# Optimization experiments

Measured on AMD Instinct MI355X. Metric: run time of the kernel, lower is better.

Reference implementation:

```python
import jax, jax.numpy as jnp
import numpy as np
from jax import lax

R = 10          # 10 iterations of (3x3x3 conv > 0) == one binary box dilation of radius 10
TOP_N = 250
SMOOTH = 1e-5
WEIGHT_CE = 1.0
WEIGHT_DICE = 1.0
FR_WEIGHT = 5.0


def _box_dilate(mask, r=R):
    # binary dilation with a (2r+1)^3 box, done separably along D,H,W
    x = mask.astype(jnp.float32)
    for axis in (1, 2, 3):
        win = [1, 1, 1, 1]
        win[axis] = 2 * r + 1
        x = lax.reduce_window(x, 0.0, lax.max, tuple(win), (1, 1, 1, 1), 'SAME')
    return x > 0


def _masked_mean(x, mask):
    cnt = jnp.sum(mask)
    s = jnp.sum(jnp.where(mask, x, 0.0))
    return jnp.where(cnt > 0, s / jnp.maximum(cnt, 1), 0.0)


def _fr_loss(feature, label):
    pos = label[:, 0] == 1                                  # (B,D,H,W)
    neg = label[:, 0] == 0
    f = jnp.moveaxis(feature, 1, -1)                        # (B,D,H,W,C)
    cnt = jnp.sum(pos)
    # mean positive feature (zeros if no positives)
    mean_pos = jnp.sum(jnp.where(pos[..., None], f, 0.0), axis=(0, 1, 2, 3)) / jnp.maximum(cnt, 1)
    std_feat = jnp.where(cnt > 0, mean_pos, 0.0)
    std_n = std_feat / jnp.maximum(jnp.linalg.norm(std_feat), 1e-12)
    # normalized feature map; cosine of a normalized feature with std_n == dot product
    f_n = f / jnp.maximum(jnp.linalg.norm(f, axis=-1, keepdims=True), 1e-12)
    cos_map = jnp.einsum('bdhwc,c->bdhw', f_n, std_n)
    # 1) positive compactness loss
    positive_loss = _masked_mean(1.0 - cos_map, pos)
    easy = _box_dilate(pos) & (~pos)
    mis_loss = _masked_mean(jax.nn.relu(cos_map), easy)
    # 3) hardest negatives: top-250 negative similarities, scatter to mask, dilate
    neg_sims = jnp.where(neg, cos_map, -1e30).reshape(-1)
    top_v, top_i = lax.top_k(neg_sims, TOP_N)
    hi = jnp.zeros(neg_sims.shape, jnp.float32).at[top_i].set((top_v > -1e29).astype(jnp.float32))
    hi = hi.reshape(pos.shape) > 0
    final_neg = _box_dilate(hi) & (~pos)
    neg_loss = _masked_mean(jax.nn.relu(cos_map), final_neg)
    return positive_loss + mis_loss + neg_loss


def _ce_and_dice(net_output, target):
    C = net_output.shape[1]
    logp = jax.nn.log_softmax(net_output, axis=1)           # (B,C,D,H,W)
    ce = -jnp.mean(jnp.take_along_axis(logp, target, axis=1))
    p = jnp.exp(logp)
    y = jax.nn.one_hot(target[:, 0], C, dtype=p.dtype)      # (B,D,H,W,C)
    y = jnp.moveaxis(y, -1, 1)                               # (B,C,D,H,W)
    axes = (0, 2, 3, 4)                                      # batch_dice=True
    tp = jnp.sum(p * y, axes)
    fp = jnp.sum(p * (1.0 - y), axes)
    fn = jnp.sum((1.0 - p) * y, axes)
    dc = (2.0 * tp + SMOOTH) / jnp.maximum(2.0 * tp + fp + fn + SMOOTH, 1e-8)
    dc_loss = -jnp.mean(dc[1:])                              # do_bg=False
    return ce, dc_loss


def setup_inputs() -> dict:
    key = jax.random.key(0)
    k1, k2, k3 = jax.random.split(key, 3)
    B, Cf, Cls, S = 2, 16, 3, 128
    feature = jax.random.normal(k1, (B, Cf, S, S, S), dtype=jnp.float32)
    net_output = jax.random.normal(k2, (B, Cls, S, S, S), dtype=jnp.float32)
    target = jax.random.randint(k3, (B, 1, S, S, S), 0, 3, dtype=jnp.int32)
    return {"feature": feature, "net_output": net_output, "target": target}


def reference(feature, net_output, target):
    ce, dc = _ce_and_dice(net_output, target)
    fr = _fr_loss(feature, target)
    return WEIGHT_CE * ce + WEIGHT_DICE * dc + FR_WEIGHT * fr
```

## Files before the change

kernel.cpp:

```cpp
#include <hip/hip_runtime.h>
#include <hip/hip_bf16.h>
#include <math.h>

#define S3    128
#define NB    2
#define CF    16
#define CHS   (S3*S3*S3)
#define NVOX  (NB*CHS)
#define NW    (NVOX/64)
#define CAP   1048576

typedef unsigned long long u64;
typedef unsigned int u32;
typedef float f4 __attribute__((ext_vector_type(4)));
typedef int   i4 __attribute__((ext_vector_type(4)));

#define ACC_OFF    0
#define STD_OFF    512
#define SCAN_OFF   576
#define HIST_OFF   1024
#define HIB_OFF    (HIST_OFF + 4096*4)
#define ZERO_BYTES (HIB_OFF + NW*8)
#define POSB_OFF   544768
#define NEGB_OFF   (POSB_OFF + NW*8)
#define DTMP_OFF   (NEGB_OFF + NW*8)
#define CAND_OFF   (DTMP_OFF + 2*NW*8)
#define COS_OFF    (CAND_OFF + CAP*8)


__device__ __forceinline__ double wave_red(double x) {
    for (int o = 32; o > 0; o >>= 1) x += __shfl_down(x, o);
    return x;
}
__device__ __forceinline__ u32 mono_key(float f) {
    u32 u = __float_as_uint(f);
    return (u & 0x80000000u) ? ~u : (u | 0x80000000u);
}
__device__ __forceinline__ u64 spread4(u32 x16) {
    u64 x = (u64)(x16 & 0xFFFFu);
    x = (x | (x << 24)) & 0x000000FF000000FFull;
    x = (x | (x << 12)) & 0x000F000F000F000Full;
    x = (x | (x << 6))  & 0x0303030303030303ull;
    x = (x | (x << 3))  & 0x1111111111111111ull;
    return x;
}

template<int NBINS>
__device__ __forceinline__ void sel_desc(const u32* h, u32 need, u32* ss, u32* res)
{
    const int t = threadIdx.x;
    const int CH = NBINS / 256;
    u32 s = 0;
    #pragma unroll
    for (int j = 0; j < CH; j++) s += h[t * CH + j];
    ss[t] = s;
    __syncthreads();
    for (int o = 1; o < 256; o <<= 1) {
        u32 v = (t + o < 256) ? ss[t + o] : 0;
        __syncthreads();
        ss[t] += v;
        __syncthreads();
    }
    u32 above = ss[t] - s;
    if (above < need && above + s >= need) {
        u32 cum = above;
        int bin = t * CH;
        for (int b = t * CH + CH - 1; b >= t * CH; b--) {
            if (cum + h[b] >= need) { bin = b; break; }
            cum += h[b];
        }
        res[0] = (u32)bin;
        res[1] = need - cum;
    }
    __syncthreads();
}

__global__ __launch_bounds__(256) void k_main(const float* __restrict__ feat,
        const float* __restrict__ net, const int* __restrict__ tgt,
        u64* __restrict__ posb, u64* __restrict__ negb, double* __restrict__ acc)
{
    int tid = blockIdx.x * 256 + threadIdx.x;
    const int gstride = gridDim.x * 256;
    const int lane = threadIdx.x & 63;
    float fs[16];
    #pragma unroll
    for (int c = 0; c < 16; c++) fs[c] = 0.f;
    float ce = 0.f, s0 = 0.f, s1 = 0.f, s2 = 0.f, ta0 = 0.f, ta1 = 0.f, ta2 = 0.f;
    int n0 = 0, n1 = 0, n2 = 0;

    for (int idx = tid; idx < NVOX / 4; idx += gstride) {
        const int v4 = idx << 2;
        const int b = v4 >> 21;
        const i4 tv = __builtin_nontemporal_load((const i4*)(tgt + v4));
        const int T[4] = {tv[0], tv[1], tv[2], tv[3]};
        u32 nib_p = (u32)(T[0]==1) | ((u32)(T[1]==1)<<1) | ((u32)(T[2]==1)<<2) | ((u32)(T[3]==1)<<3);
        u32 nib_n = (u32)(T[0]==0) | ((u32)(T[1]==0)<<1) | ((u32)(T[2]==0)<<2) | ((u32)(T[3]==0)<<3);
        int pp = __popc(nib_p), nn_ = __popc(nib_n);
        n1 += pp; n0 += nn_; n2 += 4 - pp - nn_;

        u64 bp0 = __ballot(nib_p & 1), bp1 = __ballot(nib_p & 2),
            bp2 = __ballot(nib_p & 4), bp3 = __ballot(nib_p & 8);
        u64 bn0 = __ballot(nib_n & 1), bn1 = __ballot(nib_n & 2),
            bn2 = __ballot(nib_n & 4), bn3 = __ballot(nib_n & 8);
        if ((lane & 15) == 0) {
            int wsel = lane >> 4, sh = wsel << 4;
            u64 wp = spread4((u32)(bp0 >> sh)) | (spread4((u32)(bp1 >> sh)) << 1)
                   | (spread4((u32)(bp2 >> sh)) << 2) | (spread4((u32)(bp3 >> sh)) << 3);
            u64 wn = spread4((u32)(bn0 >> sh)) | (spread4((u32)(bn1 >> sh)) << 1)
                   | (spread4((u32)(bn2 >> sh)) << 2) | (spread4((u32)(bn3 >> sh)) << 3);
            int wi = ((idx - lane) >> 4) + wsel;
            posb[wi] = wp; negb[wi] = wn;
        }

        const size_t nbase = (size_t)v4 + (size_t)b * (2u * CHS);
        f4 a0 = __builtin_nontemporal_load((const f4*)(net + nbase));
        f4 a1 = __builtin_nontemporal_load((const f4*)(net + nbase + CHS));
        f4 a2 = __builtin_nontemporal_load((const f4*)(net + nbase + 2 * (size_t)CHS));
        #pragma unroll
        for (int j = 0; j < 4; j++) {
            float x0 = a0[j], x1 = a1[j], x2 = a2[j];
            float m = fmaxf(x0, fmaxf(x1, x2));
            float e0 = expf(x0 - m), e1 = expf(x1 - m), e2 = expf(x2 - m);
            float sum = e0 + e1 + e2;
            float lse = m + logf(sum);
            int t = T[j];
            float xt = (t == 0) ? x0 : ((t == 1) ? x1 : x2);
            ce += lse - xt;
            float inv = 1.f / sum;
            float p0 = e0 * inv, p1 = e1 * inv, p2 = e2 * inv;
            s0 += p0; s1 += p1; s2 += p2;
            if (t == 0) ta0 += p0; else if (t == 1) ta1 += p1; else ta2 += p2;
        }

        if (nib_p) {
            const float* fb = feat + (size_t)v4 + (size_t)b * ((size_t)(CF - 1) * CHS);
            float w0 = (float)(nib_p & 1), w1 = (float)((nib_p >> 1) & 1),
                  w2 = (float)((nib_p >> 2) & 1), w3 = (float)((nib_p >> 3) & 1);
            #pragma unroll
            for (int c = 0; c < 16; c++) {
                float4 f = *(const float4*)(fb + (size_t)c * CHS);
                fs[c] += f.x * w0 + f.y * w1 + f.z * w2 + f.w * w3;
            }
        }
    }

    __shared__ double red[4][26];
    double vals[26];
    #pragma unroll
    for (int c = 0; c < 16; c++) vals[c] = (double)fs[c];
    vals[16] = n0; vals[17] = n1; vals[18] = n2;
    vals[19] = ce; vals[20] = s0; vals[21] = s1; vals[22] = s2;
    vals[23] = ta0; vals[24] = ta1; vals[25] = ta2;
    int wid = threadIdx.x >> 6;
    #pragma unroll
    for (int i = 0; i < 26; i++) {
        double x = wave_red(vals[i]);
        if (lane == 0) red[wid][i] = x;
    }
    __syncthreads();
    if (threadIdx.x < 26) {
        double s = red[0][threadIdx.x] + red[1][threadIdx.x] + red[2][threadIdx.x] + red[3][threadIdx.x];
        atomicAdd(&acc[threadIdx.x], s);
    }
}

__global__ void k_std(const double* __restrict__ acc, float* __restrict__ stdn) {
    __shared__ float v[16];
    double cnt = acc[17];
    if (threadIdx.x < 16) {
        double mp = acc[threadIdx.x] / fmax(cnt, 1.0);
        v[threadIdx.x] = (cnt > 0.0) ? (float)mp : 0.0f;
    }
    __syncthreads();
    if (threadIdx.x == 0) {
        float n = 0;
        for (int c = 0; c < 16; c++) n += v[c] * v[c];
        n = fmaxf(sqrtf(n), 1e-12f);
        for (int c = 0; c < 16; c++) stdn[c] = v[c] / n;
    }
}

__global__ __launch_bounds__(256) void k_cos(const float* __restrict__ feat,
        const float* __restrict__ stdn, const u64* __restrict__ negb,
        float* __restrict__ cosm, u32* __restrict__ hist)
{
    __shared__ u32 h[4096];
    __shared__ float sn[16];
    for (int i = threadIdx.x; i < 4096; i += 256) h[i] = 0;
    if (threadIdx.x < 16) sn[threadIdx.x] = stdn[threadIdx.x];
    __syncthreads();
    int tid = blockIdx.x * 256 + threadIdx.x;
    const int gstride = gridDim.x * 256;
    for (int idx = tid; idx < NVOX / 4; idx += gstride) {
        const int v4 = idx << 2;
        const int b = v4 >> 21;
        const float* fb = feat + (size_t)v4 + (size_t)b * ((size_t)(CF - 1) * CHS);
        float d0 = 0, d1 = 0, d2 = 0, d3 = 0, q0 = 0, q1 = 0, q2 = 0, q3 = 0;
        #pragma unroll
        for (int c = 0; c < 16; c++) {
            float4 f = *(const float4*)(fb + (size_t)c * CHS);
            float s = sn[c];
            d0 = fmaf(f.x, s, d0); q0 = fmaf(f.x, f.x, q0);
            d1 = fmaf(f.y, s, d1); q1 = fmaf(f.y, f.y, q1);
            d2 = fmaf(f.z, s, d2); q2 = fmaf(f.z, f.z, q2);
            d3 = fmaf(f.w, s, d3); q3 = fmaf(f.w, f.w, q3);
        }
        f4 cv;
        cv[0] = d0 / fmaxf(sqrtf(q0), 1e-12f);
        cv[1] = d1 / fmaxf(sqrtf(q1), 1e-12f);
        cv[2] = d2 / fmaxf(sqrtf(q2), 1e-12f);
        cv[3] = d3 / fmaxf(sqrtf(q3), 1e-12f);
        __builtin_nontemporal_store(cv, (f4*)(cosm + v4));
        u32 nib = (u32)(negb[v4 >> 6] >> (v4 & 63)) & 0xFu;
        if (nib & 1) atomicAdd(&h[mono_key(cv[0]) >> 20], 1u);
        if (nib & 2) atomicAdd(&h[mono_key(cv[1]) >> 20], 1u);
        if (nib & 4) atomicAdd(&h[mono_key(cv[2]) >> 20], 1u);
        if (nib & 8) atomicAdd(&h[mono_key(cv[3]) >> 20], 1u);
    }
    __syncthreads();
    for (int i = threadIdx.x; i < 4096; i += 256)
        if (h[i]) atomicAdd(&hist[i], h[i]);
}

__global__ __launch_bounds__(256) void k_scanA(const u32* __restrict__ hist, u32* __restrict__ scan) {
    __shared__ u32 h[4096];
    __shared__ u32 ss[256];
    __shared__ u32 res[2];
    for (int i = threadIdx.x; i < 4096; i += 256) h[i] = hist[i];
    __syncthreads();
    sel_desc<4096>(h, 250u, ss, res);
    if (threadIdx.x == 0) { scan[0] = res[0]; scan[1] = res[1]; }
}

__global__ __launch_bounds__(256) void k_collect(const float* __restrict__ cosm,
        const u64* __restrict__ negb, u32* __restrict__ scan, u64* __restrict__ cand)
{
    const u32 thr = scan[0] << 20;
    int tid = blockIdx.x * 256 + threadIdx.x;
    const int gstride = gridDim.x * 256;
    for (int idx = tid; idx < NVOX / 4; idx += gstride) {
        const int v4 = idx << 2;
        u32 nib = (u32)(negb[v4 >> 6] >> (v4 & 63)) & 0xFu;
        if (!nib) continue;
        float4 cv = *(const float4*)(cosm + v4);
        const float C[4] = {cv.x, cv.y, cv.z, cv.w};
        #pragma unroll
        for (int j = 0; j < 4; j++) {
            if ((nib >> j) & 1) {
                u32 key = mono_key(C[j]);
                if (key >= thr) {
                    u32 p = atomicAdd(&scan[4], 1u);
                    if (p < CAP) cand[p] = ((u64)key << 32) | (u32)(v4 + j);
                }
            }
        }
    }
}

__global__ __launch_bounds__(256) void k_select(const u64* __restrict__ cand,
        const u32* __restrict__ scan, u64* __restrict__ hib)
{
    __shared__ u32 h[4096];
    __shared__ u32 ss[256];
    __shared__ u32 res[2];
    __shared__ u32 eqlist[2048];
    __shared__ u32 eqc;
    const u32 cnt = scan[4];
    const int n = (int)(cnt < CAP ? cnt : CAP);
    const u32 binA = scan[0];
    const u32 need1 = scan[1];

    for (int i = threadIdx.x; i < 4096; i += 256) h[i] = 0;
    if (threadIdx.x == 0) eqc = 0;
    __syncthreads();
    for (int i = threadIdx.x; i < n; i += 256) {
        u32 key = (u32)(cand[i] >> 32);
        if ((key >> 20) == binA) atomicAdd(&h[(key >> 8) & 0xFFFu], 1u);
    }
    __syncthreads();
    sel_desc<4096>(h, need1, ss, res);
    const u32 b1 = res[0], need2 = res[1];

    for (int i = threadIdx.x; i < 4096; i += 256) h[i] = 0;
    __syncthreads();
    const u32 pre24 = (binA << 12) | b1;
    for (int i = threadIdx.x; i < n; i += 256) {
        u32 key = (u32)(cand[i] >> 32);
        if ((key >> 8) == pre24) atomicAdd(&h[key & 0xFFu], 1u);
    }
    __syncthreads();
    sel_desc<256>(h, need2, ss, res);
    const u32 K = (pre24 << 8) | res[0];
    const u32 need3 = res[1];

    for (int i = threadIdx.x; i < n; i += 256) {
        u64 code = cand[i];
        u32 key = (u32)(code >> 32), vi = (u32)code;
        if (key > K) atomicOr(&hib[vi >> 6], 1ull << (vi & 63));
        else if (key == K) { u32 p = atomicAdd(&eqc, 1u); if (p < 2048) eqlist[p] = vi; }
    }
    __syncthreads();
    if (threadIdx.x == 0) {
        int m = (int)(eqc < 2048u ? eqc : 2048u);
        u32 prev = 0; bool first = true;
        for (u32 k = 0; k < need3; k++) {
            u32 best = 0xFFFFFFFFu;
            for (int i = 0; i < m; i++) {
                u32 x = eqlist[i];
                if ((first || x > prev) && x < best) best = x;
            }
            if (best == 0xFFFFFFFFu) break;
            atomicOr(&hib[best >> 6], 1ull << (best & 63));
            prev = best; first = false;
        }
    }
}

__global__ __launch_bounds__(256) void k_dilD(const u64* __restrict__ posb,
        const u64* __restrict__ hib, u64* __restrict__ dtmp)
{
    int t = blockIdx.x * 256 + threadIdx.x;
    int m = t >> 16, wI = t & 65535;
    const u64* in = m ? hib : posb;
    int dd = (wI >> 8) & 127;
    int base = wI - (dd << 8);
    int lo = dd > 10 ? dd - 10 : 0, hi2 = dd + 10 > 127 ? 127 : dd + 10;
    u64 r = 0;
    for (int j = lo; j <= hi2; j++) r |= in[base + (j << 8)];
    dtmp[t] = r;
}

__global__ __launch_bounds__(256) void k_dilfin(const u64* __restrict__ dtmp,
        const u64* __restrict__ posb, const float* __restrict__ cosm,
        double* __restrict__ acc)
{
    __shared__ u64 A0[256], A1[256], B0[256], B1[256], E[256], F[256], P[256];
    __shared__ double red[4][5];
    const int s = blockIdx.x;
    const int t = threadIdx.x;
    const int sbase = s * 256;
    A0[t] = dtmp[sbase + t];
    A1[t] = dtmp[65536 + sbase + t];
    P[t]  = posb[sbase + t];
    __syncthreads();
    {
        int hh = t >> 1, col = t & 1;
        int lo = hh > 10 ? hh - 10 : 0, hi2 = hh + 10 > 127 ? 127 : hh + 10;
        u64 r0 = 0, r1 = 0;
        for (int j = lo; j <= hi2; j++) { r0 |= A0[(j << 1) + col]; r1 |= A1[(j << 1) + col]; }
        B0[t] = r0; B1[t] = r1;
    }
    __syncthreads();
    if (t < 128) {
        u64 lo0 = B0[t * 2], hi0 = B0[t * 2 + 1];
        u64 lo1 = B1[t * 2], hi1 = B1[t * 2 + 1];
        u64 rl0 = lo0, rh0 = hi0, rl1 = lo1, rh1 = hi1;
        #pragma unroll
        for (int sft = 1; sft <= 10; sft++) {
            rl0 |= (lo0 << sft) | (lo0 >> sft) | (hi0 << (64 - sft));
            rh0 |= (hi0 << sft) | (hi0 >> sft) | (lo0 >> (64 - sft));
            rl1 |= (lo1 << sft) | (lo1 >> sft) | (hi1 << (64 - sft));
            rh1 |= (hi1 << sft) | (hi1 >> sft) | (lo1 >> (64 - sft));
        }
        E[t * 2] = rl0; E[t * 2 + 1] = rh0;
        F[t * 2] = rl1; F[t * 2 + 1] = rh1;
    }
    __syncthreads();
    float sp = 0.f, se = 0.f, sf = 0.f;
    int cE = 0, cF = 0;
    const float* cbase = cosm + (size_t)s * 16384;
    #pragma unroll 4
    for (int i = 0; i < 16; i++) {
        int q = t + 256 * i;
        int lw = q >> 4, sh = (q & 15) * 4;
        u64 pw = P[lw];
        u32 np_ = (u32)(pw >> sh) & 0xFu;
        u32 ne  = (u32)((E[lw] & ~pw) >> sh) & 0xFu;
        u32 nf  = (u32)((F[lw] & ~pw) >> sh) & 0xFu;
        if (!(np_ | ne | nf)) continue;
        f4 cv = __builtin_nontemporal_load((const f4*)(cbase + q * 4));
        #pragma unroll
        for (int j = 0; j < 4; j++) {
            float cs = cv[j], rl = fmaxf(cs, 0.f);
            if ((np_ >> j) & 1) sp += 1.f - cs;
            if ((ne >> j) & 1) { se += rl; cE++; }
            if ((nf >> j) & 1) { sf += rl; cF++; }
        }
    }
    int lane = t & 63, wid = t >> 6;
    double vals[5] = {(double)sp, (double)se, (double)cE, (double)sf, (double)cF};
    #pragma unroll
    for (int i = 0; i < 5; i++) {
        double x = wave_red(vals[i]);
        if (lane == 0) red[wid][i] = x;
    }
    __syncthreads();
    if (t < 5) {
        double sum = red[0][t] + red[1][t] + red[2][t] + red[3][t];
        atomicAdd(&acc[26 + t], sum);
    }
}

__global__ void k_combine(const double* __restrict__ acc, float* __restrict__ out) {
    if (threadIdx.x != 0 || blockIdx.x != 0) return;
    double ce = acc[19] / (double)NVOX;
    double dcl = 0;
    for (int c = 1; c <= 2; c++) {
        double T = acc[23 + c], S = acc[20 + c], N = acc[16 + c];
        dcl += (2.0 * T + 1e-5) / fmax(S + N + 1e-5, 1e-8);
    }
    double dc_loss = -(dcl / 2.0);
    double cnt = acc[17];
    double pl = (cnt > 0.0) ? acc[26] / fmax(cnt, 1.0) : 0.0;
    double ml = (acc[28] > 0.0) ? acc[27] / acc[28] : 0.0;
    double nl = (acc[30] > 0.0) ? acc[29] / acc[30] : 0.0;
    out[0] = (float)(ce + dc_loss + 5.0 * (pl + ml + nl));
}

extern "C" void kernel_launch(void* const* d_in, const int* in_sizes, int n_in,
                              void* d_out, int out_size, void* d_ws, size_t ws_size,
                              hipStream_t stream)
{
    const float* feat = (const float*)d_in[0];
    const float* net  = (const float*)d_in[1];
    const int*   tgt  = (const int*)d_in[2];
    float* out = (float*)d_out;
    char* w = (char*)d_ws;

    double* acc  = (double*)(w + ACC_OFF);
    float* stdn  = (float*)(w + STD_OFF);
    u32* scan    = (u32*)(w + SCAN_OFF);
    u32* hist    = (u32*)(w + HIST_OFF);
    u64* hib     = (u64*)(w + HIB_OFF);
    u64* posb    = (u64*)(w + POSB_OFF);
    u64* negb    = (u64*)(w + NEGB_OFF);
    u64* dtmp    = (u64*)(w + DTMP_OFF);
    u64* cand    = (u64*)(w + CAND_OFF);
    float* cosm  = (float*)(w + COS_OFF);

    hipMemsetAsync(w, 0, ZERO_BYTES, stream);

    k_main   <<<2048, 256, 0, stream>>>(feat, net, tgt, posb, negb, acc);
    k_std    <<<1,    64,  0, stream>>>(acc, stdn);
    k_cos    <<<2048, 256, 0, stream>>>(feat, stdn, negb, cosm, hist);
    k_scanA  <<<1,    256, 0, stream>>>(hist, scan);
    k_collect<<<2048, 256, 0, stream>>>(cosm, negb, scan, cand);
    k_select <<<1,    256, 0, stream>>>(cand, scan, hib);
    k_dilD   <<<512,  256, 0, stream>>>(posb, hib, dtmp);
    k_dilfin <<<256,  256, 0, stream>>>(dtmp, posb, cosm, acc);
    k_combine<<<1,    64,  0, stream>>>(acc, out);
}
```

Baseline: 197.6 us.

## Split positive-feature sum out of main kernel into separate dense pass

Splits the fused main kernel into a CE/dice/bitmask kernel and a separate kernel that sums positive-voxel features using the posb bitmask with branch-free weights. The goal is to remove the divergent conditional 16-channel feature loads and the register pressure of the fused kernel. In exchange it adds a kernel launch, and the new kernel reads all feature data unconditionally instead of only groups containing positives. With about a third of voxels positive, nearly every group was loading features anyway.

```diff
diff --git a/kernel.cpp b/kernel.cpp
--- a/kernel.cpp
+++ b/kernel.cpp
@@ -75,16 +75,13 @@
     __syncthreads();
 }
 
-__global__ __launch_bounds__(256) void k_main(const float* __restrict__ feat,
-        const float* __restrict__ net, const int* __restrict__ tgt,
-        u64* __restrict__ posb, u64* __restrict__ negb, double* __restrict__ acc)
+__global__ __launch_bounds__(256) void k_ce(const float* __restrict__ net,
+        const int* __restrict__ tgt, u64* __restrict__ posb, u64* __restrict__ negb,
+        double* __restrict__ acc)
 {
     int tid = blockIdx.x * 256 + threadIdx.x;
     const int gstride = gridDim.x * 256;
     const int lane = threadIdx.x & 63;
-    float fs[16];
-    #pragma unroll
-    for (int c = 0; c < 16; c++) fs[c] = 0.f;
     float ce = 0.f, s0 = 0.f, s1 = 0.f, s2 = 0.f, ta0 = 0.f, ta1 = 0.f, ta2 = 0.f;
     int n0 = 0, n1 = 0, n2 = 0;
 
@@ -131,34 +128,58 @@
             s0 += p0; s1 += p1; s2 += p2;
             if (t == 0) ta0 += p0; else if (t == 1) ta1 += p1; else ta2 += p2;
         }
-
-        if (nib_p) {
-            const float* fb = feat + (size_t)v4 + (size_t)b * ((size_t)(CF - 1) * CHS);
-            float w0 = (float)(nib_p & 1), w1 = (float)((nib_p >> 1) & 1),
-                  w2 = (float)((nib_p >> 2) & 1), w3 = (float)((nib_p >> 3) & 1);
-            #pragma unroll
-            for (int c = 0; c < 16; c++) {
-                float4 f = *(const float4*)(fb + (size_t)c * CHS);
-                fs[c] += f.x * w0 + f.y * w1 + f.z * w2 + f.w * w3;
-            }
-        }
-    }
-
-    __shared__ double red[4][26];
-    double vals[26];
-    #pragma unroll
-    for (int c = 0; c < 16; c++) vals[c] = (double)fs[c];
-    vals[16] = n0; vals[17] = n1; vals[18] = n2;
-    vals[19] = ce; vals[20] = s0; vals[21] = s1; vals[22] = s2;
-    vals[23] = ta0; vals[24] = ta1; vals[25] = ta2;
+    }
+
+    __shared__ double red[4][10];
+    double vals[10] = {(double)n0, (double)n1, (double)n2, (double)ce,
+                       (double)s0, (double)s1, (double)s2,
+                       (double)ta0, (double)ta1, (double)ta2};
     int wid = threadIdx.x >> 6;
     #pragma unroll
-    for (int i = 0; i < 26; i++) {
+    for (int i = 0; i < 10; i++) {
         double x = wave_red(vals[i]);
         if (lane == 0) red[wid][i] = x;
     }
     __syncthreads();
-    if (threadIdx.x < 26) {
+    if (threadIdx.x < 10) {
+        double s = red[0][threadIdx.x] + red[1][threadIdx.x] + red[2][threadIdx.x] + red[3][threadIdx.x];
+        atomicAdd(&acc[16 + threadIdx.x], s);
+    }
+}
+
+__global__ __launch_bounds__(256) void k_pos(const float* __restrict__ feat,
+        const u64* __restrict__ posb, double* __restrict__ acc)
+{
+    int tid = blockIdx.x * 256 + threadIdx.x;
+    const int gstride = gridDim.x * 256;
+    const int lane = threadIdx.x & 63;
+    float fs[16];
+    #pragma unroll
+    for (int c = 0; c < 16; c++) fs[c] = 0.f;
+
+    for (int idx = tid; idx < NVOX / 4; idx += gstride) {
+        const int v4 = idx << 2;
+        const int b = v4 >> 21;
+        u32 nib = (u32)(posb[v4 >> 6] >> (v4 & 63)) & 0xFu;
+        float w0 = (float)(nib & 1), w1 = (float)((nib >> 1) & 1),
+              w2 = (float)((nib >> 2) & 1), w3 = (float)((nib >> 3) & 1);
+        const float* fb = feat + (size_t)v4 + (size_t)b * ((size_t)(CF - 1) * CHS);
+        #pragma unroll
+        for (int c = 0; c < 16; c++) {
+            f4 f = *(const f4*)(fb + (size_t)c * CHS);
+            fs[c] += f[0] * w0 + f[1] * w1 + f[2] * w2 + f[3] * w3;
+        }
+    }
+
+    __shared__ double red[4][16];
+    int wid = threadIdx.x >> 6;
+    #pragma unroll
+    for (int i = 0; i < 16; i++) {
+        double x = wave_red((double)fs[i]);
+        if (lane == 0) red[wid][i] = x;
+    }
+    __syncthreads();
+    if (threadIdx.x < 16) {
         double s = red[0][threadIdx.x] + red[1][threadIdx.x] + red[2][threadIdx.x] + red[3][threadIdx.x];
         atomicAdd(&acc[threadIdx.x], s);
     }
@@ -198,12 +219,12 @@
         float d0 = 0, d1 = 0, d2 = 0, d3 = 0, q0 = 0, q1 = 0, q2 = 0, q3 = 0;
         #pragma unroll
         for (int c = 0; c < 16; c++) {
-            float4 f = *(const float4*)(fb + (size_t)c * CHS);
+            f4 f = *(const f4*)(fb + (size_t)c * CHS);
             float s = sn[c];
-            d0 = fmaf(f.x, s, d0); q0 = fmaf(f.x, f.x, q0);
-            d1 = fmaf(f.y, s, d1); q1 = fmaf(f.y, f.y, q1);
-            d2 = fmaf(f.z, s, d2); q2 = fmaf(f.z, f.z, q2);
-            d3 = fmaf(f.w, s, d3); q3 = fmaf(f.w, f.w, q3);
+            d0 = fmaf(f[0], s, d0); q0 = fmaf(f[0], f[0], q0);
+            d1 = fmaf(f[1], s, d1); q1 = fmaf(f[1], f[1], q1);
+            d2 = fmaf(f[2], s, d2); q2 = fmaf(f[2], f[2], q2);
+            d3 = fmaf(f[3], s, d3); q3 = fmaf(f[3], f[3], q3);
         }
         f4 cv;
         cv[0] = d0 / fmaxf(sqrtf(q0), 1e-12f);
@@ -440,7 +461,8 @@
 
     hipMemsetAsync(w, 0, ZERO_BYTES, stream);
 
-    k_main   <<<2048, 256, 0, stream>>>(feat, net, tgt, posb, negb, acc);
+    k_ce     <<<2048, 256, 0, stream>>>(net, tgt, posb, negb, acc);
+    k_pos    <<<1024, 256, 0, stream>>>(feat, posb, acc);
     k_std    <<<1,    64,  0, stream>>>(acc, stdn);
     k_cos    <<<2048, 256, 0, stream>>>(feat, stdn, negb, cosm, hist);
     k_scanA  <<<1,    256, 0, stream>>>(hist, scan);
```

Measured after the change: 207.0 us. 1.05x slower.
